# Optimization experiments

Measured on AMD Instinct MI355X. Metric: run time of the kernel, lower is better.

The kernel has to match this reference:

```python
import jax, jax.numpy as jnp
import numpy as np

B, ORDER, N, D, H = 16, 2, 512, 128, 8
DH = D // H
NEG_SLOPE = 0.2


def setup_inputs() -> dict:
    key = jax.random.key(0)
    ks = jax.random.split(key, 8)
    stdv = 1.0 / np.sqrt(DH)

    def u(k, shape):
        return jax.random.uniform(k, shape, jnp.float32, -stdv, stdv)

    x = jax.random.normal(ks[0], (B, ORDER, N, D), jnp.float32)
    A = jax.random.randint(ks[1], (B, ORDER, N, N), 0, 5, jnp.int32)
    # Stacked params for the 2*order GAT modules: axis0 = order, axis1 = (conv1, conv2)
    W = u(ks[2], (ORDER, 2, D, D))            # project.weight
    pb = jnp.zeros((ORDER, 2, D), jnp.float32)  # project.bias (init 0)
    att_src = u(ks[3], (ORDER, 2, H, DH))
    att_dst = u(ks[4], (ORDER, 2, H, DH))
    bias = jnp.zeros((ORDER, 2, D), jnp.float32)  # GAT output bias (init 0)
    return {"x": x, "A": A, "W": W, "pb": pb,
            "att_src": att_src, "att_dst": att_dst, "bias": bias}


def _gat(x, Af, W, pb, a_src, a_dst, b):
    # x: [B,N,D]; Af: [B,N,N] float in {0,1}
    xp = x @ W.T + pb                                  # project
    xh = xp.reshape(B, N, H, DH)                       # [B,N,H,DH]
    s_src = jnp.einsum('bnhd,hd->bnh', xh, a_src)      # [B,N,H]
    s_dst = jnp.einsum('bnhd,hd->bnh', xh, a_dst)
    alpha = s_src[:, :, None, :] + s_dst[:, None, :, :]  # [B,src,dst,H]
    alpha = jnp.where((Af != 1.0)[..., None], 0.0, alpha)
    alpha = jnp.where(alpha >= 0, alpha, NEG_SLOPE * alpha)  # leaky relu
    alpha = jax.nn.softmax(alpha, axis=1)              # softmax over src dim
    out = jnp.einsum('bsdh,bshf->bdhf', alpha, xh).reshape(B, N, D)
    out = out + xp                                     # add_self_loops
    return out + b


def reference(x, A, W, pb, att_src, att_dst, bias):
    A1 = ((A == 2) | (A == 4)).astype(x.dtype)  # [B,ORDER,N,N]
    A2 = ((A == 3) | (A == 4)).astype(x.dtype)
    hs = []
    for i in range(ORDER):
        h1 = _gat(x[:, i], A1[:, i], W[i, 0], pb[i, 0], att_src[i, 0], att_dst[i, 0], bias[i, 0])
        h2 = _gat(x[:, i], A2[:, i], W[i, 1], pb[i, 1], att_src[i, 1], att_dst[i, 1], bias[i, 1])
        hs.append(h1 + h2)
    h = jnp.stack(hs, axis=1)                          # [B,ORDER,N,D]
    out = h + h.mean(axis=1, keepdims=True)
    return out
```

## Files before the change

### kernel.cpp

```cpp
#include <hip/hip_runtime.h>

#define N_ 512
#define D_ 128
#define LOG2E 1.44269504088896f


typedef __attribute__((ext_vector_type(8))) short short8;
typedef __attribute__((ext_vector_type(4))) float floatx4;
typedef __attribute__((ext_vector_type(4))) unsigned int uintx4;

#if defined(__has_builtin)
#if __has_builtin(__builtin_amdgcn_exp2f)
#define EXP2F(x) __builtin_amdgcn_exp2f(x)
#else
#define EXP2F(x) exp2f(x)
#endif
#else
#define EXP2F(x) exp2f(x)
#endif

__device__ __forceinline__ unsigned short f2bf(float f) {
    unsigned int u = __float_as_uint(f);
    u += 0x7fffu + ((u >> 16) & 1u);
    return (unsigned short)(u >> 16);
}
__device__ __forceinline__ float bflo(unsigned int u) { return __uint_as_float(u << 16); }
__device__ __forceinline__ float bfhi(unsigned int u) { return __uint_as_float(u & 0xffff0000u); }

__global__ __launch_bounds__(256) void prep_kernel(
    const float* __restrict__ x, const float* __restrict__ W,
    const float* __restrict__ pb, const float* __restrict__ att_src,
    const float* __restrict__ att_dst, const int* __restrict__ A,
    unsigned short* __restrict__ xpt, unsigned int* __restrict__ sgE,
    float2* __restrict__ sgD, unsigned short* __restrict__ mg)
{
    const int bid0 = blockIdx.x;
    const int t = threadIdx.x;

    if (bid0 >= 1024) {
        const int bid = bid0 - 1024;
        const int stile = bid & 31;
        const int bi = bid >> 5;
        const int sl = t >> 4, lane = t & 15;
        const int s = stile * 16 + sl;
        const int* Ar = A + ((size_t)bi * N_ + s) * N_ + lane * 32;
        unsigned int m0 = 0, m1 = 0;
#pragma unroll
        for (int g = 0; g < 8; ++g) {
            const int4 v = *(const int4*)(Ar + g * 4);
            const int k = g * 4;
            if (v.x == 2 || v.x == 4) m0 |= 1u << (k + 0);
            if (v.x == 3 || v.x == 4) m1 |= 1u << (k + 0);
            if (v.y == 2 || v.y == 4) m0 |= 1u << (k + 1);
            if (v.y == 3 || v.y == 4) m1 |= 1u << (k + 1);
            if (v.z == 2 || v.z == 4) m0 |= 1u << (k + 2);
            if (v.z == 3 || v.z == 4) m1 |= 1u << (k + 2);
            if (v.w == 2 || v.w == 4) m0 |= 1u << (k + 3);
            if (v.w == 3 || v.w == 4) m1 |= 1u << (k + 3);
        }
        const size_t b0 = ((size_t)bi * 2 + 0) * 32 * N_;
        const size_t b1 = ((size_t)bi * 2 + 1) * 32 * N_;
        const int T0 = lane * 2, T1 = lane * 2 + 1;
        mg[b0 + (size_t)T0 * N_ + s] = (unsigned short)(m0 & 0xFFFFu);
        mg[b0 + (size_t)T1 * N_ + s] = (unsigned short)(m0 >> 16);
        mg[b1 + (size_t)T0 * N_ + s] = (unsigned short)(m1 & 0xFFFFu);
        mg[b1 + (size_t)T1 * N_ + s] = (unsigned short)(m1 >> 16);
        return;
    }

    const int unit = bid0 >> 1;
    const int half = bid0 & 1;
    const int ntile = unit & 7;
    const int inst  = unit >> 3;
    const int j = inst & 1;
    const int bi = inst >> 1;
    const int ij = (bi & 1) * 2 + j;
    const int wave = t >> 6, L = t & 63, n = L & 15, q = L >> 4;

    const int n0w = ntile * 64 + wave * 16;
    const float* xrow = x + ((size_t)bi * N_ + n0w + n) * D_ + q * 8;
    short8 Af[4];
#pragma unroll
    for (int kc = 0; kc < 4; ++kc) {
        const float4 a0 = *(const float4*)(xrow + kc * 32);
        const float4 a1 = *(const float4*)(xrow + kc * 32 + 4);
        uintx4 au;
        au.x = f2bf(a0.x) | ((unsigned int)f2bf(a0.y) << 16);
        au.y = f2bf(a0.z) | ((unsigned int)f2bf(a0.w) << 16);
        au.z = f2bf(a1.x) | ((unsigned int)f2bf(a1.y) << 16);
        au.w = f2bf(a1.z) | ((unsigned int)f2bf(a1.w) << 16);
        Af[kc] = __builtin_bit_cast(short8, au);
    }

    const float* wb = W + (size_t)ij * D_ * D_;
#pragma unroll
    for (int ft = 0; ft < 4; ++ft) {
        const int head = half * 4 + ft;
        const int fg = head * 16 + n;
        const float* wrow = wb + (size_t)fg * D_ + q * 8;
        floatx4 C = (floatx4){0.f, 0.f, 0.f, 0.f};
#pragma unroll
        for (int kc = 0; kc < 4; ++kc) {
            const float4 b0 = *(const float4*)(wrow + kc * 32);
            const float4 b1 = *(const float4*)(wrow + kc * 32 + 4);
            uintx4 bu;
            bu.x = f2bf(b0.x) | ((unsigned int)f2bf(b0.y) << 16);
            bu.y = f2bf(b0.z) | ((unsigned int)f2bf(b0.w) << 16);
            bu.z = f2bf(b1.x) | ((unsigned int)f2bf(b1.y) << 16);
            bu.w = f2bf(b1.z) | ((unsigned int)f2bf(b1.w) << 16);
            C = __builtin_amdgcn_mfma_f32_16x16x32_bf16(
                Af[kc], __builtin_bit_cast(short8, bu), C, 0, 0, 0);
        }
        const float pbv = pb[ij * D_ + fg];
        float xp0 = C[0] + pbv, xp1 = C[1] + pbv;
        float xp2 = C[2] + pbv, xp3 = C[3] + pbv;
        uint2 pk;
        pk.x = f2bf(xp0) | ((unsigned int)f2bf(xp1) << 16);
        pk.y = f2bf(xp2) | ((unsigned int)f2bf(xp3) << 16);
        *(uint2*)&xpt[((size_t)inst * D_ + fg) * N_ + n0w + q * 4] = pk;

        const float asv = att_src[ij * D_ + fg];
        const float adv = att_dst[ij * D_ + fg];
        float sa0 = xp0 * asv, sa1 = xp1 * asv, sa2 = xp2 * asv, sa3 = xp3 * asv;
        float sb0 = xp0 * adv, sb1 = xp1 * adv, sb2 = xp2 * adv, sb3 = xp3 * adv;
#pragma unroll
        for (int off = 1; off < 16; off <<= 1) {
            sa0 += __shfl_xor(sa0, off); sa1 += __shfl_xor(sa1, off);
            sa2 += __shfl_xor(sa2, off); sa3 += __shfl_xor(sa3, off);
            sb0 += __shfl_xor(sb0, off); sb1 += __shfl_xor(sb1, off);
            sb2 += __shfl_xor(sb2, off); sb3 += __shfl_xor(sb3, off);
        }
        if (n < 4) {
            const float v = ((n == 0) ? sa0 : (n == 1) ? sa1 : (n == 2) ? sa2 : sa3) * LOG2E;
            const unsigned int pkv = f2bf(EXP2F(v)) |
                ((unsigned int)f2bf(EXP2F(0.2f * v)) << 16);
            sgE[((size_t)inst * 8 + head) * N_ + n0w + q * 4 + n] = pkv;
        } else if (n >= 8 && n < 12) {
            const int r = n - 8;
            const float v = ((r == 0) ? sb0 : (r == 1) ? sb1 : (r == 2) ? sb2 : sb3) * LOG2E;
            float2 ed;
            ed.x = EXP2F(v);
            ed.y = EXP2F(0.2f * v);
            sgD[((size_t)inst * 8 + head) * N_ + n0w + q * 4 + r] = ed;
        }
    }
}

__global__ __launch_bounds__(256) void attn_kernel(
    const unsigned short* __restrict__ xpt,
    const unsigned int* __restrict__ sgE,
    const float2* __restrict__ sgD,
    const unsigned short* __restrict__ mg,
    const float* __restrict__ bias,
    float* __restrict__ hout)
{
    __shared__ unsigned int es_l[8 * N_];
    __shared__ unsigned short mask_l[N_];

    const int bid = blockIdx.x;
    const int tile = bid & 31;
    const int cj   = (bid >> 5) & 1;
    const int bi   = bid >> 6;
    const int inst = bi * 2 + cj;
    const int ij = (bi & 1) * 2 + cj;
    const int d0 = tile * 16;
    const int t = threadIdx.x;
    const int wave = t >> 6, L = t & 63, n = L & 15, q = L >> 4;
    const int h0 = wave * 2;
    const int n16 = n + 16;

    {
        const uint4* src = (const uint4*)(sgE + (size_t)inst * 8 * N_);
        uint4* dst = (uint4*)es_l;
#pragma unroll
        for (int r = 0; r < 4; ++r) dst[r * 256 + t] = src[r * 256 + t];
    }
    if (t < 64)
        ((uint4*)mask_l)[t] =
            ((const uint4*)(mg + ((size_t)inst * 32 + tile) * N_))[t];

    float iEd[2], rd[2];
#pragma unroll
    for (int hh = 0; hh < 2; ++hh) {
        const float2 ed = sgD[((size_t)inst * 8 + h0 + hh) * N_ + d0 + n];
        iEd[hh] = 1.0f / ed.x;
        rd[hh] = ed.y * iEd[hh];
    }

    __syncthreads();

    const unsigned short* xpi = xpt + (size_t)inst * D_ * N_;

    const uintx4 ou = { 0x3F803F80u, 0x3F803F80u, 0x3F803F80u, 0x3F803F80u };
    const short8 onesB = __builtin_bit_cast(short8, ou);

    floatx4 Cacc[2] = { (floatx4){0.f,0.f,0.f,0.f}, (floatx4){0.f,0.f,0.f,0.f} };
    floatx4 Cz[2]   = { (floatx4){0.f,0.f,0.f,0.f}, (floatx4){0.f,0.f,0.f,0.f} };

    short8 Bf0 = *(const short8*)(xpi + (size_t)(h0 * 16 + n) * N_ + q * 8);
    short8 Bf1 = *(const short8*)(xpi + (size_t)((h0 + 1) * 16 + n) * N_ + q * 8);
    for (int c = 0; c < 16; ++c) {
        const int sq = c * 32 + q * 8;
        short8 nB0, nB1;
        if (c < 15) {
            nB0 = *(const short8*)(xpi + (size_t)(h0 * 16 + n) * N_ + sq + 32);
            nB1 = *(const short8*)(xpi + (size_t)((h0 + 1) * 16 + n) * N_ + sq + 32);
        }
        const uint4 mv = *(const uint4*)&mask_l[sq];
        const unsigned int mw[4] = { mv.x, mv.y, mv.z, mv.w };
#pragma unroll
        for (int hh = 0; hh < 2; ++hh) {
            const uint4 e0 = *(const uint4*)&es_l[(h0 + hh) * N_ + sq];
            const uint4 e1 = *(const uint4*)&es_l[(h0 + hh) * N_ + sq + 4];
            const unsigned int epk[8] = { e0.x, e0.y, e0.z, e0.w,
                                          e1.x, e1.y, e1.z, e1.w };
            unsigned int wt[8];
#pragma unroll
            for (int idx = 0; idx < 8; ++idx) {
                const float Es = bflo(epk[idx]);
                const float Fs = bfhi(epk[idx]);
                const float wv = fmaxf(Es, Fs * rd[hh]);
                const unsigned int bit =
                    (mw[idx >> 1] >> ((idx & 1) ? n16 : n)) & 1u;
                wt[idx] = __float_as_uint(bit ? wv : iEd[hh]);
            }
            uintx4 au;
            au.x = __builtin_amdgcn_perm(wt[1], wt[0], 0x07060302);
            au.y = __builtin_amdgcn_perm(wt[3], wt[2], 0x07060302);
            au.z = __builtin_amdgcn_perm(wt[5], wt[4], 0x07060302);
            au.w = __builtin_amdgcn_perm(wt[7], wt[6], 0x07060302);
            const short8 As = __builtin_bit_cast(short8, au);
            Cacc[hh] = __builtin_amdgcn_mfma_f32_16x16x32_bf16(
                As, hh ? Bf1 : Bf0, Cacc[hh], 0, 0, 0);
            Cz[hh] = __builtin_amdgcn_mfma_f32_16x16x32_bf16(
                As, onesB, Cz[hh], 0, 0, 0);
        }
        Bf0 = nB0;
        Bf1 = nB1;
    }

#pragma unroll
    for (int hh = 0; hh < 2; ++hh) {
        const int h = h0 + hh;
        const float bv = bias[ij * D_ + h * 16 + n];
        const uint2 sv = *(const uint2*)(xpi + (size_t)(h * 16 + n) * N_ + d0 + q * 4);
        const float selfv[4] = { bflo(sv.x), bfhi(sv.x), bflo(sv.y), bfhi(sv.y) };
#pragma unroll
        for (int reg = 0; reg < 4; ++reg) {
            const float Zi = 1.0f / Cz[hh][reg];
            const float val = Cacc[hh][reg] * Zi + selfv[reg] + bv;
            unsafeAtomicAdd(
                &hout[((size_t)bi * N_ + d0 + q * 4 + reg) * D_ + h * 16 + n], val);
        }
    }
}

__global__ __launch_bounds__(256) void combine_kernel(float* __restrict__ h)
{
    const int idx = blockIdx.x * 256 + threadIdx.x;
    const int b = idx >> 14;
    const int r = idx & 16383;
    float4* p0 = (float4*)h + (size_t)b * 32768 + r;
    float4* p1 = p0 + 16384;
    const float4 a = *p0;
    const float4 o = *p1;
    float4 r0, r1;
    r0.x = 1.5f * a.x + 0.5f * o.x;  r1.x = 1.5f * o.x + 0.5f * a.x;
    r0.y = 1.5f * a.y + 0.5f * o.y;  r1.y = 1.5f * o.y + 0.5f * a.y;
    r0.z = 1.5f * a.z + 0.5f * o.z;  r1.z = 1.5f * o.z + 0.5f * a.z;
    r0.w = 1.5f * a.w + 0.5f * o.w;  r1.w = 1.5f * o.w + 0.5f * a.w;
    *p0 = r0;
    *p1 = r1;
}

extern "C" void kernel_launch(void* const* d_in, const int* in_sizes, int n_in,
                              void* d_out, int out_size, void* d_ws, size_t ws_size,
                              hipStream_t stream)
{
    const float* x   = (const float*)d_in[0];
    const int*   A   = (const int*)d_in[1];
    const float* W   = (const float*)d_in[2];
    const float* pb  = (const float*)d_in[3];
    const float* as_ = (const float*)d_in[4];
    const float* ad_ = (const float*)d_in[5];
    const float* bs  = (const float*)d_in[6];

    unsigned short* xpt = (unsigned short*)d_ws;
    unsigned int* sgE = (unsigned int*)(xpt + (size_t)64 * D_ * N_);
    float2* sgD = (float2*)(sgE + (size_t)64 * 8 * N_);
    unsigned short* mg = (unsigned short*)(sgD + (size_t)64 * 8 * N_);
    float* h = (float*)d_out;

    hipMemsetAsync(d_out, 0, (size_t)out_size * sizeof(float), stream);
    prep_kernel<<<2048, 256, 0, stream>>>(x, W, pb, as_, ad_, A, xpt, sgE, sgD, mg);
    attn_kernel<<<2048, 256, 0, stream>>>(xpt, sgE, sgD, mg, bs, h);
    combine_kernel<<<1024, 256, 0, stream>>>(h);
}
```

Before: 161.9 us.

## Switch attention weights to packed fp16 math and register-resident transposed masks

Replaces bf16 with fp16 throughout and uses hardware pkrtz conversion instead of manual rounding. Attention-weight computation now runs on packed half2 multiply/max and a bitmask select instead of per-element float ops and perm packing. Masks are transposed in prep so each lane loads its bits once into registers instead of reading them from LDS, and the mask prep grid shrinks to 512 blocks. Narrower fp16 range could overflow the exp terms, and the precomputed E/F values lose some accuracy.

```diff
diff --git a/kernel.cpp b/kernel.cpp
--- a/kernel.cpp
+++ b/kernel.cpp
@@ -8,6 +8,8 @@
 typedef __attribute__((ext_vector_type(8))) short short8;
 typedef __attribute__((ext_vector_type(4))) float floatx4;
 typedef __attribute__((ext_vector_type(4))) unsigned int uintx4;
+typedef __attribute__((ext_vector_type(2))) _Float16 half2v;
+typedef __attribute__((ext_vector_type(8))) _Float16 half8;
 
 #if defined(__has_builtin)
 #if __has_builtin(__builtin_amdgcn_exp2f)
@@ -19,52 +21,51 @@
 #define EXP2F(x) exp2f(x)
 #endif
 
-__device__ __forceinline__ unsigned short f2bf(float f) {
-    unsigned int u = __float_as_uint(f);
-    u += 0x7fffu + ((u >> 16) & 1u);
-    return (unsigned short)(u >> 16);
-}
-__device__ __forceinline__ float bflo(unsigned int u) { return __uint_as_float(u << 16); }
-__device__ __forceinline__ float bfhi(unsigned int u) { return __uint_as_float(u & 0xffff0000u); }
+__device__ __forceinline__ unsigned int pkh(float a, float b) {
+    auto h = __builtin_amdgcn_cvt_pkrtz(a, b);
+    return __builtin_bit_cast(unsigned int, h);
+}
 
 __global__ __launch_bounds__(256) void prep_kernel(
     const float* __restrict__ x, const float* __restrict__ W,
     const float* __restrict__ pb, const float* __restrict__ att_src,
     const float* __restrict__ att_dst, const int* __restrict__ A,
-    unsigned short* __restrict__ xpt, unsigned int* __restrict__ sgE,
-    float2* __restrict__ sgD, unsigned short* __restrict__ mg)
+    unsigned short* __restrict__ xpt, unsigned int* __restrict__ sgEs,
+    unsigned int* __restrict__ sgFs, float2* __restrict__ sgD,
+    unsigned int* __restrict__ mgT)
 {
     const int bid0 = blockIdx.x;
     const int t = threadIdx.x;
 
     if (bid0 >= 1024) {
         const int bid = bid0 - 1024;
-        const int stile = bid & 31;
-        const int bi = bid >> 5;
-        const int sl = t >> 4, lane = t & 15;
-        const int s = stile * 16 + sl;
-        const int* Ar = A + ((size_t)bi * N_ + s) * N_ + lane * 32;
-        unsigned int m0 = 0, m1 = 0;
-#pragma unroll
-        for (int g = 0; g < 8; ++g) {
-            const int4 v = *(const int4*)(Ar + g * 4);
-            const int k = g * 4;
-            if (v.x == 2 || v.x == 4) m0 |= 1u << (k + 0);
-            if (v.x == 3 || v.x == 4) m1 |= 1u << (k + 0);
-            if (v.y == 2 || v.y == 4) m0 |= 1u << (k + 1);
-            if (v.y == 3 || v.y == 4) m1 |= 1u << (k + 1);
-            if (v.z == 2 || v.z == 4) m0 |= 1u << (k + 2);
-            if (v.z == 3 || v.z == 4) m1 |= 1u << (k + 2);
-            if (v.w == 2 || v.w == 4) m0 |= 1u << (k + 3);
-            if (v.w == 3 || v.w == 4) m1 |= 1u << (k + 3);
-        }
-        const size_t b0 = ((size_t)bi * 2 + 0) * 32 * N_;
-        const size_t b1 = ((size_t)bi * 2 + 1) * 32 * N_;
-        const int T0 = lane * 2, T1 = lane * 2 + 1;
-        mg[b0 + (size_t)T0 * N_ + s] = (unsigned short)(m0 & 0xFFFFu);
-        mg[b0 + (size_t)T1 * N_ + s] = (unsigned short)(m0 >> 16);
-        mg[b1 + (size_t)T0 * N_ + s] = (unsigned short)(m1 & 0xFFFFu);
-        mg[b1 + (size_t)T1 * N_ + s] = (unsigned short)(m1 >> 16);
+        const int bi = bid >> 4;
+        const int rem = bid & 15;
+        const int dg = rem >> 2;
+        const int jw = rem & 3;
+        const int dp = t & 63, q = t >> 6;
+        const int dstb = dg * 128 + dp * 2;
+        const int sbase = jw * 128 + q * 8;
+        const int* Ab = A + (size_t)bi * N_ * N_ + dstb;
+        unsigned int a00 = 0, a01 = 0, a10 = 0, a11 = 0;
+#pragma unroll
+        for (int cp = 0; cp < 4; ++cp) {
+#pragma unroll
+            for (int i = 0; i < 8; ++i) {
+                const int s = sbase + cp * 32 + i;
+                const int2 v = *(const int2*)(Ab + (size_t)s * N_);
+                const int bitp = cp * 8 + i;
+                a00 |= ((0x14u >> v.x) & 1u) << bitp;
+                a10 |= ((0x18u >> v.x) & 1u) << bitp;
+                a01 |= ((0x14u >> v.y) & 1u) << bitp;
+                a11 |= ((0x18u >> v.y) & 1u) << bitp;
+            }
+        }
+        const int i0 = bi * 2;
+        mgT[(((size_t)i0 * 4 + q) * 512 + dstb + 0) * 4 + jw] = a00;
+        mgT[(((size_t)i0 * 4 + q) * 512 + dstb + 1) * 4 + jw] = a01;
+        mgT[(((size_t)(i0 + 1) * 4 + q) * 512 + dstb + 0) * 4 + jw] = a10;
+        mgT[(((size_t)(i0 + 1) * 4 + q) * 512 + dstb + 1) * 4 + jw] = a11;
         return;
     }
 
@@ -79,17 +80,17 @@
 
     const int n0w = ntile * 64 + wave * 16;
     const float* xrow = x + ((size_t)bi * N_ + n0w + n) * D_ + q * 8;
-    short8 Af[4];
+    half8 Af[4];
 #pragma unroll
     for (int kc = 0; kc < 4; ++kc) {
         const float4 a0 = *(const float4*)(xrow + kc * 32);
         const float4 a1 = *(const float4*)(xrow + kc * 32 + 4);
         uintx4 au;
-        au.x = f2bf(a0.x) | ((unsigned int)f2bf(a0.y) << 16);
-        au.y = f2bf(a0.z) | ((unsigned int)f2bf(a0.w) << 16);
-        au.z = f2bf(a1.x) | ((unsigned int)f2bf(a1.y) << 16);
-        au.w = f2bf(a1.z) | ((unsigned int)f2bf(a1.w) << 16);
-        Af[kc] = __builtin_bit_cast(short8, au);
+        au.x = pkh(a0.x, a0.y);
+        au.y = pkh(a0.z, a0.w);
+        au.z = pkh(a1.x, a1.y);
+        au.w = pkh(a1.z, a1.w);
+        Af[kc] = __builtin_bit_cast(half8, au);
     }
 
     const float* wb = W + (size_t)ij * D_ * D_;
@@ -104,19 +105,19 @@
             const float4 b0 = *(const float4*)(wrow + kc * 32);
             const float4 b1 = *(const float4*)(wrow + kc * 32 + 4);
             uintx4 bu;
-            bu.x = f2bf(b0.x) | ((unsigned int)f2bf(b0.y) << 16);
-            bu.y = f2bf(b0.z) | ((unsigned int)f2bf(b0.w) << 16);
-            bu.z = f2bf(b1.x) | ((unsigned int)f2bf(b1.y) << 16);
-            bu.w = f2bf(b1.z) | ((unsigned int)f2bf(b1.w) << 16);
-            C = __builtin_amdgcn_mfma_f32_16x16x32_bf16(
-                Af[kc], __builtin_bit_cast(short8, bu), C, 0, 0, 0);
+            bu.x = pkh(b0.x, b0.y);
+            bu.y = pkh(b0.z, b0.w);
+            bu.z = pkh(b1.x, b1.y);
+            bu.w = pkh(b1.z, b1.w);
+            C = __builtin_amdgcn_mfma_f32_16x16x32_f16(
+                Af[kc], __builtin_bit_cast(half8, bu), C, 0, 0, 0);
         }
         const float pbv = pb[ij * D_ + fg];
         float xp0 = C[0] + pbv, xp1 = C[1] + pbv;
         float xp2 = C[2] + pbv, xp3 = C[3] + pbv;
         uint2 pk;
-        pk.x = f2bf(xp0) | ((unsigned int)f2bf(xp1) << 16);
-        pk.y = f2bf(xp2) | ((unsigned int)f2bf(xp3) << 16);
+        pk.x = pkh(xp0, xp1);
+        pk.y = pkh(xp2, xp3);
         *(uint2*)&xpt[((size_t)inst * D_ + fg) * N_ + n0w + q * 4] = pk;
 
         const float asv = att_src[ij * D_ + fg];
@@ -131,10 +132,12 @@
             sb2 += __shfl_xor(sb2, off); sb3 += __shfl_xor(sb3, off);
         }
         if (n < 4) {
-            const float v = ((n == 0) ? sa0 : (n == 1) ? sa1 : (n == 2) ? sa2 : sa3) * LOG2E;
-            const unsigned int pkv = f2bf(EXP2F(v)) |
-                ((unsigned int)f2bf(EXP2F(0.2f * v)) << 16);
-            sgE[((size_t)inst * 8 + head) * N_ + n0w + q * 4 + n] = pkv;
+            const float vlo = ((n & 1) ? sa2 : sa0) * LOG2E;
+            const float vhi = ((n & 1) ? sa3 : sa1) * LOG2E;
+            const float sc = (n < 2) ? 1.0f : 0.2f;
+            const unsigned int pkv = pkh(EXP2F(sc * vlo), EXP2F(sc * vhi));
+            unsigned int* dstp = (n < 2) ? sgEs : sgFs;
+            dstp[((size_t)inst * 8 + head) * 256 + (n0w >> 1) + q * 2 + (n & 1)] = pkv;
         } else if (n >= 8 && n < 12) {
             const int r = n - 8;
             const float v = ((r == 0) ? sb0 : (r == 1) ? sb1 : (r == 2) ? sb2 : sb3) * LOG2E;
@@ -148,14 +151,16 @@
 
 __global__ __launch_bounds__(256) void attn_kernel(
     const unsigned short* __restrict__ xpt,
-    const unsigned int* __restrict__ sgE,
+    const unsigned int* __restrict__ sgEs,
+    const unsigned int* __restrict__ sgFs,
     const float2* __restrict__ sgD,
-    const unsigned short* __restrict__ mg,
+    const unsigned int* __restrict__ mgT,
     const float* __restrict__ bias,
     float* __restrict__ hout)
 {
-    __shared__ unsigned int es_l[8 * N_];
-    __shared__ unsigned short mask_l[N_];
+    __shared__ unsigned int es_l[8 * 256];
+    __shared__ unsigned int fs_l[8 * 256];
+    __shared__ unsigned int seltab[4];
 
     const int bid = blockIdx.x;
     const int tile = bid & 31;
@@ -167,76 +172,89 @@
     const int t = threadIdx.x;
     const int wave = t >> 6, L = t & 63, n = L & 15, q = L >> 4;
     const int h0 = wave * 2;
-    const int n16 = n + 16;
 
     {
-        const uint4* src = (const uint4*)(sgE + (size_t)inst * 8 * N_);
-        uint4* dst = (uint4*)es_l;
-#pragma unroll
-        for (int r = 0; r < 4; ++r) dst[r * 256 + t] = src[r * 256 + t];
-    }
-    if (t < 64)
-        ((uint4*)mask_l)[t] =
-            ((const uint4*)(mg + ((size_t)inst * 32 + tile) * N_))[t];
-
-    float iEd[2], rd[2];
+        const uint4* sE = (const uint4*)(sgEs + (size_t)inst * 2048);
+        const uint4* sF = (const uint4*)(sgFs + (size_t)inst * 2048);
+        ((uint4*)es_l)[t]       = sE[t];
+        ((uint4*)es_l)[256 + t] = sE[256 + t];
+        ((uint4*)fs_l)[t]       = sF[t];
+        ((uint4*)fs_l)[256 + t] = sF[256 + t];
+    }
+    if (t < 4) seltab[t] = ((t & 1) ? 0x0000FFFFu : 0u) | ((t & 2) ? 0xFFFF0000u : 0u);
+
+    const uint4 mreg = *(const uint4*)(mgT + (((size_t)inst * 4 + q) * 512 + d0 + n) * 4);
+    const unsigned int mw_[4] = { mreg.x, mreg.y, mreg.z, mreg.w };
+
+    unsigned int iEd2[2], rd2[2];
 #pragma unroll
     for (int hh = 0; hh < 2; ++hh) {
         const float2 ed = sgD[((size_t)inst * 8 + h0 + hh) * N_ + d0 + n];
-        iEd[hh] = 1.0f / ed.x;
-        rd[hh] = ed.y * iEd[hh];
+        const float iEd = 1.0f / ed.x;
+        const float rdv = ed.y * iEd;
+        iEd2[hh] = pkh(iEd, iEd);
+        rd2[hh] = pkh(rdv, rdv);
     }
 
     __syncthreads();
 
     const unsigned short* xpi = xpt + (size_t)inst * D_ * N_;
-
-    const uintx4 ou = { 0x3F803F80u, 0x3F803F80u, 0x3F803F80u, 0x3F803F80u };
-    const short8 onesB = __builtin_bit_cast(short8, ou);
+    const unsigned short* bp0 = xpi + (size_t)(h0 * 16 + n) * N_;
+    const unsigned short* bp1 = xpi + (size_t)((h0 + 1) * 16 + n) * N_;
+
+    const uintx4 ou = { 0x3C003C00u, 0x3C003C00u, 0x3C003C00u, 0x3C003C00u };
+    const half8 onesB = __builtin_bit_cast(half8, ou);
 
     floatx4 Cacc[2] = { (floatx4){0.f,0.f,0.f,0.f}, (floatx4){0.f,0.f,0.f,0.f} };
     floatx4 Cz[2]   = { (floatx4){0.f,0.f,0.f,0.f}, (floatx4){0.f,0.f,0.f,0.f} };
 
-    short8 Bf0 = *(const short8*)(xpi + (size_t)(h0 * 16 + n) * N_ + q * 8);
-    short8 Bf1 = *(const short8*)(xpi + (size_t)((h0 + 1) * 16 + n) * N_ + q * 8);
+    uintx4 B0 = *(const uintx4*)(bp0 + q * 8);
+    uintx4 B1 = *(const uintx4*)(bp1 + q * 8);
+#pragma unroll
     for (int c = 0; c < 16; ++c) {
         const int sq = c * 32 + q * 8;
-        short8 nB0, nB1;
+        uintx4 nB0, nB1;
         if (c < 15) {
-            nB0 = *(const short8*)(xpi + (size_t)(h0 * 16 + n) * N_ + sq + 32);
-            nB1 = *(const short8*)(xpi + (size_t)((h0 + 1) * 16 + n) * N_ + sq + 32);
-        }
-        const uint4 mv = *(const uint4*)&mask_l[sq];
-        const unsigned int mw[4] = { mv.x, mv.y, mv.z, mv.w };
+            nB0 = *(const uintx4*)(bp0 + sq + 32);
+            nB1 = *(const uintx4*)(bp1 + sq + 32);
+        }
+        const unsigned int word = mw_[c >> 2];
+        unsigned int sel[4];
+#pragma unroll
+        for (int p = 0; p < 4; ++p) {
+            const int sh = (c & 3) * 8 + 2 * p;
+            const unsigned int b4 = (sh >= 2) ? ((word >> (sh - 2)) & 12u)
+                                              : ((word << 2) & 12u);
+            sel[p] = *(const unsigned int*)((const char*)seltab + b4);
+        }
+        const int spb = c * 16 + q * 4;
 #pragma unroll
         for (int hh = 0; hh < 2; ++hh) {
-            const uint4 e0 = *(const uint4*)&es_l[(h0 + hh) * N_ + sq];
-            const uint4 e1 = *(const uint4*)&es_l[(h0 + hh) * N_ + sq + 4];
-            const unsigned int epk[8] = { e0.x, e0.y, e0.z, e0.w,
-                                          e1.x, e1.y, e1.z, e1.w };
-            unsigned int wt[8];
-#pragma unroll
-            for (int idx = 0; idx < 8; ++idx) {
-                const float Es = bflo(epk[idx]);
-                const float Fs = bfhi(epk[idx]);
-                const float wv = fmaxf(Es, Fs * rd[hh]);
-                const unsigned int bit =
-                    (mw[idx >> 1] >> ((idx & 1) ? n16 : n)) & 1u;
-                wt[idx] = __float_as_uint(bit ? wv : iEd[hh]);
+            const uint4 Ep = *(const uint4*)&es_l[(h0 + hh) * 256 + spb];
+            const uint4 Fp = *(const uint4*)&fs_l[(h0 + hh) * 256 + spb];
+            const unsigned int eu[4] = { Ep.x, Ep.y, Ep.z, Ep.w };
+            const unsigned int fu[4] = { Fp.x, Fp.y, Fp.z, Fp.w };
+            const half2v rdh = __builtin_bit_cast(half2v, rd2[hh]);
+            uintx4 au;
+            unsigned int wts[4];
+#pragma unroll
+            for (int p = 0; p < 4; ++p) {
+                const half2v e = __builtin_bit_cast(half2v, eu[p]);
+                const half2v f = __builtin_bit_cast(half2v, fu[p]);
+                const half2v pr = f * rdh;
+                const half2v wv = __builtin_elementwise_max(pr, e);
+                const unsigned int wvu = __builtin_bit_cast(unsigned int, wv);
+                wts[p] = (sel[p] & wvu) | (~sel[p] & iEd2[hh]);
             }
-            uintx4 au;
-            au.x = __builtin_amdgcn_perm(wt[1], wt[0], 0x07060302);
-            au.y = __builtin_amdgcn_perm(wt[3], wt[2], 0x07060302);
-            au.z = __builtin_amdgcn_perm(wt[5], wt[4], 0x07060302);
-            au.w = __builtin_amdgcn_perm(wt[7], wt[6], 0x07060302);
-            const short8 As = __builtin_bit_cast(short8, au);
-            Cacc[hh] = __builtin_amdgcn_mfma_f32_16x16x32_bf16(
-                As, hh ? Bf1 : Bf0, Cacc[hh], 0, 0, 0);
-            Cz[hh] = __builtin_amdgcn_mfma_f32_16x16x32_bf16(
+            au.x = wts[0]; au.y = wts[1]; au.z = wts[2]; au.w = wts[3];
+            const half8 As = __builtin_bit_cast(half8, au);
+            Cacc[hh] = __builtin_amdgcn_mfma_f32_16x16x32_f16(
+                As, __builtin_bit_cast(half8, hh ? B1 : B0), Cacc[hh], 0, 0, 0);
+            Cz[hh] = __builtin_amdgcn_mfma_f32_16x16x32_f16(
                 As, onesB, Cz[hh], 0, 0, 0);
         }
-        Bf0 = nB0;
-        Bf1 = nB1;
+        B0 = nB0;
+        B1 = nB1;
     }
 
 #pragma unroll
@@ -244,7 +262,10 @@
         const int h = h0 + hh;
         const float bv = bias[ij * D_ + h * 16 + n];
         const uint2 sv = *(const uint2*)(xpi + (size_t)(h * 16 + n) * N_ + d0 + q * 4);
-        const float selfv[4] = { bflo(sv.x), bfhi(sv.x), bflo(sv.y), bfhi(sv.y) };
+        const half2v s0 = __builtin_bit_cast(half2v, sv.x);
+        const half2v s1 = __builtin_bit_cast(half2v, sv.y);
+        const float selfv[4] = { (float)s0[0], (float)s0[1],
+                                 (float)s1[0], (float)s1[1] };
 #pragma unroll
         for (int reg = 0; reg < 4; ++reg) {
             const float Zi = 1.0f / Cz[hh][reg];
@@ -286,13 +307,14 @@
     const float* bs  = (const float*)d_in[6];
 
     unsigned short* xpt = (unsigned short*)d_ws;
-    unsigned int* sgE = (unsigned int*)(xpt + (size_t)64 * D_ * N_);
-    float2* sgD = (float2*)(sgE + (size_t)64 * 8 * N_);
-    unsigned short* mg = (unsigned short*)(sgD + (size_t)64 * 8 * N_);
+    unsigned int* sgEs = (unsigned int*)((char*)d_ws + (8u << 20));
+    unsigned int* sgFs = (unsigned int*)((char*)d_ws + (8u << 20) + (512u << 10));
+    float2* sgD = (float2*)((char*)d_ws + (9u << 20));
+    unsigned int* mgT = (unsigned int*)((char*)d_ws + (11u << 20));
     float* h = (float*)d_out;
 
-    hipMemsetAsync(d_out, 0, (size_t)out_size * sizeof(float), stream);
-    prep_kernel<<<2048, 256, 0, stream>>>(x, W, pb, as_, ad_, A, xpt, sgE, sgD, mg);
-    attn_kernel<<<2048, 256, 0, stream>>>(xpt, sgE, sgD, mg, bs, h);
+    (void)hipMemsetAsync(d_out, 0, (size_t)out_size * sizeof(float), stream);
+    prep_kernel<<<1536, 256, 0, stream>>>(x, W, pb, as_, ad_, A, xpt, sgEs, sgFs, sgD, mgT);
+    attn_kernel<<<2048, 256, 0, stream>>>(xpt, sgEs, sgFs, sgD, mgT, bs, h);
     combine_kernel<<<1024, 256, 0, stream>>>(h);
 }
```

New measurement: 152.5 us. 1.06x faster.
